# Kernel tuning notes

Measured on AMD Instinct MI355X. Metric: run time of the kernel, lower is better.

Reference implementation:

```python
import jax, jax.numpy as jnp
import numpy as np
import math

B = 50        # graphs per batch
NPG = 2000    # nodes per graph
EPG = 12000   # edges per graph
F_IN = 256
NHID = 128
RATIO = 0.8


def setup_inputs() -> dict:
    key = jax.random.key(0)
    ks = jax.random.split(key, 12)
    N = B * NPG
    src_loc = jax.random.randint(ks[0], (B, EPG), 0, NPG)
    dst_loc = jax.random.randint(ks[1], (B, EPG), 0, NPG)
    off = (jnp.arange(B) * NPG)[:, None]
    edge_index = jnp.stack([(src_loc + off).reshape(-1), (dst_loc + off).reshape(-1)]).astype(jnp.int32)

    def lin(k, fi, fo):
        return (jax.random.normal(k, (fi, fo), jnp.float32) / np.sqrt(fi).astype(np.float32))

    return {
        "x": jax.random.normal(ks[2], (N, F_IN), jnp.float32),
        "W1": lin(ks[3], F_IN, NHID), "b1": jnp.zeros(NHID, jnp.float32),
        "Ws1": lin(ks[4], NHID, 1), "bs1": jnp.zeros(1, jnp.float32),
        "W2": lin(ks[5], NHID, NHID), "b2": jnp.zeros(NHID, jnp.float32),
        "Ws2": lin(ks[6], NHID, 1), "bs2": jnp.zeros(1, jnp.float32),
        "W3": lin(ks[7], NHID, NHID), "b3": jnp.zeros(NHID, jnp.float32),
        "Ws3": lin(ks[8], NHID, 1), "bs3": jnp.zeros(1, jnp.float32),
        "Wl": lin(ks[9], 2 * NHID, NHID), "bl": jnp.zeros(NHID, jnp.float32),
        "edge_index": edge_index,
    }


def gcn_conv(x, W, b, src, dst, w, N):
    # PyG GCNConv: D^{-1/2} (A + I) D^{-1/2} X W + b, deg from edge weights + self loop
    h = x @ W
    deg = jax.ops.segment_sum(w, dst, num_segments=N) + 1.0
    dis = jax.lax.rsqrt(deg)
    norm = w * dis[src] * dis[dst]                       # [E]
    agg = jax.ops.segment_sum(h[src] * norm[:, None], dst, num_segments=N)
    return agg + h / deg[:, None] + b                    # self-loop norm = 1/deg


def sag_pool(x, src, dst, w, Ws, bs, n_per_graph):
    N = x.shape[0]
    k = math.ceil(RATIO * n_per_graph)
    score = gcn_conv(x, Ws, bs, src, dst, w, N)[:, 0]    # [N]
    _, topi = jax.lax.top_k(score.reshape(B, n_per_graph), k)
    perm = (topi + (jnp.arange(B) * n_per_graph)[:, None]).reshape(-1)
    x_new = x[perm] * jnp.tanh(score[perm])[:, None]
    # filter_adj: keep edges whose endpoints survive, reindex; dropped edges -> weight 0
    mapping = jnp.full((N,), -1, jnp.int32).at[perm].set(jnp.arange(B * k, dtype=jnp.int32))
    ns, nd = mapping[src], mapping[dst]
    valid = (ns >= 0) & (nd >= 0) & (w > 0)
    return (x_new, jnp.where(valid, ns, 0), jnp.where(valid, nd, 0),
            jnp.where(valid, w, jnp.zeros((), x.dtype)), k)


def readout(x, n):
    # global max pool || global mean pool (equal-size graphs, nodes grouped per graph)
    xr = x.reshape(B, n, -1)
    return jnp.concatenate([xr.max(axis=1), xr.mean(axis=1)], axis=-1)


def reference(x, W1, b1, Ws1, bs1, W2, b2, Ws2, bs2, W3, b3, Ws3, bs3, Wl, bl, edge_index):
    src, dst = edge_index[0], edge_index[1]
    w = jnp.ones(src.shape[0], x.dtype)
    n = NPG
    x = jax.nn.relu(gcn_conv(x, W1, b1, src, dst, w, B * n))
    x, src, dst, w, n = sag_pool(x, src, dst, w, Ws1, bs1, n)
    x1 = readout(x, n)
    x = jax.nn.relu(gcn_conv(x, W2, b2, src, dst, w, B * n))
    x, src, dst, w, n = sag_pool(x, src, dst, w, Ws2, bs2, n)
    x2 = readout(x, n)
    x = jax.nn.relu(gcn_conv(x, W3, b3, src, dst, w, B * n))
    x, src, dst, w, n = sag_pool(x, src, dst, w, Ws3, bs3, n)
    x3 = readout(x, n)
    return jax.nn.relu((x1 + x2 + x3) @ Wl + bl)
```

## Files before the change

kernel.cpp:

```cpp
#include <hip/hip_runtime.h>
#include <math.h>

#define B_GRAPHS 50
#define NPG0     2000
#define EPG      12000
#define F_IN_C   256
#define NHID     128
#define N0       (B_GRAPHS * NPG0)
#define NE       (B_GRAPHS * EPG)
#define RSEG     16
#define GSLOTS   7
#define CPAD     136

typedef _Float16 f16x8 __attribute__((ext_vector_type(8)));
typedef float    f32x4 __attribute__((ext_vector_type(4)));

static inline int cdiv(int a, int b) { return (a + b - 1) / b; }

__global__ void k_fill_start(int* __restrict__ cnt, float* __restrict__ accum) {
    int i = blockIdx.x * 256 + threadIdx.x;
    if (i < N0) cnt[i] = 0;
    if (i < B_GRAPHS * 256) accum[i] = 0.f;
}

__global__ void k_init_edges(const int* __restrict__ ei, int* __restrict__ esrc,
                             int* __restrict__ edst, float* __restrict__ ew,
                             int* __restrict__ cnt) {
    int e = blockIdx.x * 256 + threadIdx.x;
    if (e < NE) {
        int d = ei[NE + e];
        esrc[e] = ei[e]; edst[e] = d; ew[e] = 1.0f;
        atomicAdd(&cnt[d], 1);
    }
}

__global__ void k_cvt_all(const float* __restrict__ W1, const float* __restrict__ W2,
                          const float* __restrict__ W3, _Float16* __restrict__ WT1,
                          _Float16* __restrict__ WT2, _Float16* __restrict__ WT3) {
    int t = blockIdx.x * 256 + threadIdx.x;
    if (t < 128 * 256) {
        int n = t >> 8, kk = t & 255;
        WT1[t] = (_Float16)W1[kk * 128 + n];
    } else if (t < 128 * 256 + 128 * 128) {
        int u = t - 32768; int n = u >> 7, kk = u & 127;
        WT2[u] = (_Float16)W2[kk * 128 + n];
    } else {
        int u = t - 49152; int n = u >> 7, kk = u & 127;
        WT3[u] = (_Float16)W3[kk * 128 + n];
    }
}

template<int FP32IN, int F, int GATHER>
__global__ __launch_bounds__(256) void k_gemm_ws(const void* __restrict__ Xin,
                                                 const _Float16* __restrict__ WT,
                                                 const int* __restrict__ perm,
                                                 const float* __restrict__ gate,
                                                 _Float16* __restrict__ H, int N) {
    constexpr int SMEMSZ = (F * 128 > 128 * CPAD) ? F * 128 : 128 * CPAD;
    __shared__ _Float16 smem[SMEMSZ];
    const int tid  = threadIdx.x;
    const int wave = tid >> 6, lane = tid & 63;
    const int quad = lane >> 4, l16 = lane & 15;
    const int m_blk = blockIdx.x * 128;

    constexpr int K8 = F / 8;
#pragma unroll
    for (int c = tid; c < 128 * K8; c += 256) {
        int n = c / K8, k8 = c - n * K8;
        f16x8 v = *(const f16x8*)&WT[(size_t)c * 8];
        *(f16x8*)&smem[n * F + ((k8 ^ (n & 7)) << 3)] = v;
    }
    __syncthreads();

    f32x4 acc[2][8];
#pragma unroll
    for (int i = 0; i < 2; ++i)
#pragma unroll
        for (int j = 0; j < 8; ++j) acc[i][j] = {0.f, 0.f, 0.f, 0.f};

    int row0 = m_blk + wave * 32 + l16;
    int row1 = row0 + 16;
    if (row0 > N - 1) row0 = N - 1;
    if (row1 > N - 1) row1 = N - 1;
    _Float16 g0 = (_Float16)1.0f, g1 = (_Float16)1.0f;
    if (GATHER) {
        g0 = (_Float16)gate[row0]; g1 = (_Float16)gate[row1];
        row0 = perm[row0]; row1 = perm[row1];
    }
    const int sx = l16 & 7;
    constexpr int NKQ = F / 32;

    if (FP32IN) {
        constexpr int PD = (NKQ < 4) ? NKQ : 4;
        const float* base0 = (const float*)Xin + (size_t)row0 * F + quad * 8;
        const float* base1 = (const float*)Xin + (size_t)row1 * F + quad * 8;
        float4 p0[PD][2], p1[PD][2];
#pragma unroll
        for (int i = 0; i < PD; ++i) {
            p0[i][0] = ((const float4*)(base0 + i * 32))[0];
            p0[i][1] = ((const float4*)(base0 + i * 32))[1];
            p1[i][0] = ((const float4*)(base1 + i * 32))[0];
            p1[i][1] = ((const float4*)(base1 + i * 32))[1];
        }
#pragma unroll
        for (int kq = 0; kq < NKQ; ++kq) {
            const int b = kq % PD;
            float4 f0 = p0[b][0], f1 = p0[b][1], h0 = p1[b][0], h1 = p1[b][1];
            if (kq + PD < NKQ) {
                p0[b][0] = ((const float4*)(base0 + (kq + PD) * 32))[0];
                p0[b][1] = ((const float4*)(base0 + (kq + PD) * 32))[1];
                p1[b][0] = ((const float4*)(base1 + (kq + PD) * 32))[0];
                p1[b][1] = ((const float4*)(base1 + (kq + PD) * 32))[1];
            }
            f16x8 af0 = (f16x8){(_Float16)f0.x,(_Float16)f0.y,(_Float16)f0.z,(_Float16)f0.w,
                                (_Float16)f1.x,(_Float16)f1.y,(_Float16)f1.z,(_Float16)f1.w};
            f16x8 af1 = (f16x8){(_Float16)h0.x,(_Float16)h0.y,(_Float16)h0.z,(_Float16)h0.w,
                                (_Float16)h1.x,(_Float16)h1.y,(_Float16)h1.z,(_Float16)h1.w};
            f16x8 bf[8];
#pragma unroll
            for (int j = 0; j < 8; ++j)
                bf[j] = *(const f16x8*)&smem[(j * 16 + l16) * F + ((((kq << 2) + quad) ^ sx) << 3)];
#pragma unroll
            for (int j = 0; j < 8; ++j) {
                acc[0][j] = __builtin_amdgcn_mfma_f32_16x16x32_f16(af0, bf[j], acc[0][j], 0, 0, 0);
                acc[1][j] = __builtin_amdgcn_mfma_f32_16x16x32_f16(af1, bf[j], acc[1][j], 0, 0, 0);
            }
        }
    } else {
        const _Float16* base0 = (const _Float16*)Xin + (size_t)row0 * F + quad * 8;
        const _Float16* base1 = (const _Float16*)Xin + (size_t)row1 * F + quad * 8;
        f16x8 q0[NKQ], q1[NKQ];
#pragma unroll
        for (int i = 0; i < NKQ; ++i) {
            q0[i] = *(const f16x8*)(base0 + i * 32);
            q1[i] = *(const f16x8*)(base1 + i * 32);
        }
#pragma unroll
        for (int kq = 0; kq < NKQ; ++kq) {
            f16x8 af0 = q0[kq], af1 = q1[kq];
            if (GATHER) { af0 = af0 * g0; af1 = af1 * g1; }
            f16x8 bf[8];
#pragma unroll
            for (int j = 0; j < 8; ++j)
                bf[j] = *(const f16x8*)&smem[(j * 16 + l16) * F + ((((kq << 2) + quad) ^ sx) << 3)];
#pragma unroll
            for (int j = 0; j < 8; ++j) {
                acc[0][j] = __builtin_amdgcn_mfma_f32_16x16x32_f16(af0, bf[j], acc[0][j], 0, 0, 0);
                acc[1][j] = __builtin_amdgcn_mfma_f32_16x16x32_f16(af1, bf[j], acc[1][j], 0, 0, 0);
            }
        }
    }
    __syncthreads();

    _Float16* sC = smem;
    const int rw = wave * 32;
#pragma unroll
    for (int i = 0; i < 2; ++i)
#pragma unroll
        for (int j = 0; j < 8; ++j)
#pragma unroll
            for (int g = 0; g < 4; ++g)
                sC[(rw + i * 16 + quad * 4 + g) * CPAD + j * 16 + l16] = (_Float16)acc[i][j][g];
    __syncthreads();
    {
        int rr = tid >> 1;
        int gr = m_blk + rr;
        if (gr < N) {
            _Float16* Hr = H + (size_t)gr * 128 + (tid & 1) * 64;
            const _Float16* Sr = sC + rr * CPAD + (tid & 1) * 64;
#pragma unroll
            for (int c = 0; c < 8; ++c)
                *(f16x8*)&Hr[c * 8] = *(const f16x8*)&Sr[c * 8];
        }
    }
}

__global__ __launch_bounds__(256) void k_scan(const int* __restrict__ cnt,
                                              int* __restrict__ offs,
                                              int* __restrict__ cursor, int npg) {
    __shared__ int ch[256];
    int b = blockIdx.x, tid = threadIdx.x;
    int per = (npg + 255) >> 8;
    int base = b * npg;
    int s0 = tid * per;
    int s1 = s0 + per; if (s1 > npg) s1 = npg; if (s0 > npg) s0 = npg;
    int s = 0;
    for (int i = s0; i < s1; ++i) s += cnt[base + i];
    ch[tid] = s;
    __syncthreads();
    for (int d = 1; d < 256; d <<= 1) {
        int t = ch[tid] + ((tid >= d) ? ch[tid - d] : 0);
        __syncthreads();
        ch[tid] = t;
        __syncthreads();
    }
    int run = b * EPG + ch[tid] - s;
    for (int i = s0; i < s1; ++i) {
        offs[base + i] = run; cursor[base + i] = run;
        run += cnt[base + i];
    }
}

__global__ void k_fill_csr(const int* __restrict__ esrc, const int* __restrict__ edst,
                           const float* __restrict__ ew, const int* __restrict__ cnt,
                           int* __restrict__ cursor, int* __restrict__ csr_src,
                           float* __restrict__ csr_norm) {
    int e = blockIdx.x * 256 + threadIdx.x;
    if (e < NE) {
        if (ew[e] > 0.f) {
            int sN = esrc[e], d = edst[e];
            int pos = atomicAdd(&cursor[d], 1);
            csr_src[pos] = sN;
            csr_norm[pos] = rsqrtf((float)(cnt[sN] + 1)) * rsqrtf((float)(cnt[d] + 1));
        }
    }
}

__global__ __launch_bounds__(256) void k_agg(const _Float16* __restrict__ H,
                                             const int* __restrict__ csr_src,
                                             const float* __restrict__ csr_norm,
                                             const int* __restrict__ offs,
                                             const int* __restrict__ cnt,
                                             const float* __restrict__ bias,
                                             const float* __restrict__ Ws,
                                             _Float16* __restrict__ X,
                                             float* __restrict__ hs,
                                             int bpg, int npg) {
    int bi = blockIdx.x;
    int x = bi & 7, s = bi >> 3;
    int gslot = s / bpg, blk = s - gslot * bpg;
    int g = x + 8 * gslot;
    if (g >= B_GRAPHS) return;
    int node = g * npg + blk * 4 + (threadIdx.x >> 6);
    int lane = threadIdx.x & 63;
    int quad = lane >> 4, l16 = lane & 15;

    int st = offs[node], c = cnt[node], en = st + c;
    float acc[8];
#pragma unroll
    for (int j = 0; j < 8; ++j) acc[j] = 0.f;

    if (c > 0) {
        for (int e0 = st; e0 < en; e0 += 8) {
            int eA = e0 + quad, eB = eA + 4;
            int ecA = eA < en ? eA : en - 1;
            int ecB = eB < en ? eB : en - 1;
            int uA = csr_src[ecA], uB = csr_src[ecB];
            float nA = (eA < en) ? csr_norm[ecA] : 0.f;
            float nB = (eB < en) ? csr_norm[ecB] : 0.f;
            f16x8 hA = *(const f16x8*)&H[(size_t)uA * NHID + l16 * 8];
            f16x8 hB = *(const f16x8*)&H[(size_t)uB * NHID + l16 * 8];
#pragma unroll
            for (int j = 0; j < 8; ++j) acc[j] = fmaf((float)hA[j], nA, acc[j]);
#pragma unroll
            for (int j = 0; j < 8; ++j) acc[j] = fmaf((float)hB[j], nB, acc[j]);
        }
    }
#pragma unroll
    for (int j = 0; j < 8; ++j) {
        acc[j] += __shfl_xor(acc[j], 16, 64);
        acc[j] += __shfl_xor(acc[j], 32, 64);
    }
    float invd = 1.f / (float)(c + 1);
    f16x8 hn = *(const f16x8*)&H[(size_t)node * NHID + l16 * 8];
    float4 b0 = *(const float4*)&bias[l16 * 8];
    float4 b1 = *(const float4*)&bias[l16 * 8 + 4];
    float4 w0 = *(const float4*)&Ws[l16 * 8];
    float4 w1 = *(const float4*)&Ws[l16 * 8 + 4];
    const float bb[8] = {b0.x, b0.y, b0.z, b0.w, b1.x, b1.y, b1.z, b1.w};
    const float ww[8] = {w0.x, w0.y, w0.z, w0.w, w1.x, w1.y, w1.z, w1.w};
    float sd = 0.f;
    f16x8 o;
#pragma unroll
    for (int j = 0; j < 8; ++j) {
        float v = fmaxf(acc[j] + (float)hn[j] * invd + bb[j], 0.f);
        o[j] = (_Float16)v;
        sd = fmaf(v, ww[j], sd);
    }
    if (quad == 0)
        *(f16x8*)&X[(size_t)node * NHID + l16 * 8] = o;
    sd += __shfl_xor(sd, 1, 64);
    sd += __shfl_xor(sd, 2, 64);
    sd += __shfl_xor(sd, 4, 64);
    sd += __shfl_xor(sd, 8, 64);
    if (lane == 0) hs[node] = sd;
}

__global__ void k_score(const float* __restrict__ hs, const int* __restrict__ csr_src,
                        const float* __restrict__ csr_norm, const int* __restrict__ offs,
                        const int* __restrict__ cnt, const float* __restrict__ bs,
                        float* __restrict__ score, int N) {
    int i = blockIdx.x * 256 + threadIdx.x;
    if (i >= N) return;
    int s = offs[i], c = cnt[i];
    float a = 0.f;
    for (int e = s; e < s + c; ++e) a = fmaf(hs[csr_src[e]], csr_norm[e], a);
    score[i] = a + hs[i] / (float)(c + 1) + bs[0];
}

__global__ __launch_bounds__(1024) void k_topk(const float* __restrict__ score,
                                               int* __restrict__ mapping,
                                               int* __restrict__ perm,
                                               float* __restrict__ gate,
                                               int* __restrict__ cntN,
                                               int npg, int k) {
    __shared__ float ss[2048];
    __shared__ int   si[2048];
    int b = blockIdx.x, tid = threadIdx.x;
    for (int i = tid; i < 2048; i += 1024) {
        if (i < npg) { ss[i] = score[b * npg + i]; si[i] = i; }
        else         { ss[i] = -__builtin_inff();  si[i] = i; }
    }
    __syncthreads();
    for (int size = 2; size <= 2048; size <<= 1) {
        for (int stride = size >> 1; stride > 0; stride >>= 1) {
            int t = tid;
            int i = ((t & ~(stride - 1)) << 1) | (t & (stride - 1));
            int j = i | stride;
            float sa = ss[i], sb = ss[j];
            int   ia = si[i], ib = si[j];
            bool b_before_a = (sb > sa) || (sb == sa && ib < ia);
            bool forward = ((i & size) == 0);
            bool doswap = forward ? b_before_a : !b_before_a;
            if (doswap) { ss[i] = sb; ss[j] = sa; si[i] = ib; si[j] = ia; }
            __syncthreads();
        }
    }
    for (int j = tid; j < npg; j += 1024) {
        int oldg = b * npg + si[j];
        if (j < k) {
            int newg = b * k + j;
            perm[newg] = oldg;
            mapping[oldg] = newg;
            gate[newg] = tanhf(ss[j]);
        } else {
            mapping[oldg] = -1;
        }
    }
    for (int j = tid; j < k; j += 1024) cntN[b * k + j] = 0;
}

__global__ __launch_bounds__(128) void k_pool_readout(const _Float16* __restrict__ X,
                                                      const float* __restrict__ gate,
                                                      const int* __restrict__ perm,
                                                      float* __restrict__ pmax,
                                                      float* __restrict__ psum, int k) {
    int s = blockIdx.x, b = blockIdx.y, f = threadIdx.x;
    int j0 = (k * s) / RSEG, j1 = (k * (s + 1)) / RSEG;
    float mx = -__builtin_inff(), sm = 0.f;
    for (int j = j0; j < j1; ++j) {
        int g = b * k + j;
        int old = perm[g];
        float v = (float)X[(size_t)old * NHID + f] * gate[g];
        mx = fmaxf(mx, v);
        sm += v;
    }
    pmax[(size_t)(b * RSEG + s) * NHID + f] = mx;
    psum[(size_t)(b * RSEG + s) * NHID + f] = sm;
}

__global__ __launch_bounds__(128) void k_readout_comb(const float* __restrict__ pmax,
                                                      const float* __restrict__ psum,
                                                      float* __restrict__ accum, int k) {
    int b = blockIdx.x, f = threadIdx.x;
    float mx = -__builtin_inff(), sm = 0.f;
#pragma unroll
    for (int s = 0; s < RSEG; ++s) {
        mx = fmaxf(mx, pmax[(size_t)(b * RSEG + s) * NHID + f]);
        sm += psum[(size_t)(b * RSEG + s) * NHID + f];
    }
    accum[b * 256 + f]       += mx;
    accum[b * 256 + 128 + f] += sm / (float)k;
}

__global__ void k_remap(int* __restrict__ esrc, int* __restrict__ edst,
                        float* __restrict__ ew, const int* __restrict__ mapping,
                        int* __restrict__ cntN) {
    int e = blockIdx.x * 256 + threadIdx.x;
    if (e >= NE) return;
    int sN = esrc[e], d = edst[e];
    float we = ew[e];
    int ns = mapping[sN], nd = mapping[d];
    bool valid = (ns >= 0) && (nd >= 0) && (we > 0.f);
    esrc[e] = valid ? ns : 0;
    edst[e] = valid ? nd : 0;
    ew[e] = valid ? we : 0.f;
    if (valid) atomicAdd(&cntN[nd], 1);
}

__global__ __launch_bounds__(128) void k_comb_final(const float* __restrict__ pmax,
                                                    const float* __restrict__ psum,
                                                    const float* __restrict__ accum,
                                                    const float* __restrict__ Wl,
                                                    const float* __restrict__ bl,
                                                    float* __restrict__ out, int k) {
    __shared__ float a[256];
    int b = blockIdx.x, f = threadIdx.x;
    float mx = -__builtin_inff(), sm = 0.f;
#pragma unroll
    for (int s = 0; s < RSEG; ++s) {
        mx = fmaxf(mx, pmax[(size_t)(b * RSEG + s) * NHID + f]);
        sm += psum[(size_t)(b * RSEG + s) * NHID + f];
    }
    a[f]       = accum[b * 256 + f] + mx;
    a[128 + f] = accum[b * 256 + 128 + f] + sm / (float)k;
    __syncthreads();
    float s = bl[f];
    for (int i = 0; i < 256; ++i) s = fmaf(a[i], Wl[i * NHID + f], s);
    out[b * NHID + f] = fmaxf(s, 0.f);
}

extern "C" void kernel_launch(void* const* d_in, const int* in_sizes, int n_in,
                              void* d_out, int out_size, void* d_ws, size_t ws_size,
                              hipStream_t stream) {
    const float* x0 = (const float*)d_in[0];
    const float* Wm[3] = {(const float*)d_in[1], (const float*)d_in[5], (const float*)d_in[9]};
    const float* bm[3] = {(const float*)d_in[2], (const float*)d_in[6], (const float*)d_in[10]};
    const float* Wsc[3] = {(const float*)d_in[3], (const float*)d_in[7], (const float*)d_in[11]};
    const float* bsc[3] = {(const float*)d_in[4], (const float*)d_in[8], (const float*)d_in[12]};
    const float* Wl = (const float*)d_in[13];
    const float* bl = (const float*)d_in[14];
    const int*   ei = (const int*)d_in[15];
    float* out = (float*)d_out;

    _Float16* bufA = (_Float16*)d_ws;
    _Float16* bufB = bufA + (size_t)N0 * NHID;
    _Float16* WT1  = bufB + (size_t)N0 * NHID;
    _Float16* WT2  = WT1 + 128 * 256;
    _Float16* WT3  = WT2 + 128 * 128;
    float* hs     = (float*)(WT3 + 128 * 128);
    float* score  = hs + N0;
    float* gate   = score + N0;
    float* accum  = gate + N0;
    float* pmax   = accum + B_GRAPHS * 256;
    float* psum   = pmax + B_GRAPHS * RSEG * NHID;
    int*   cntA   = (int*)(psum + B_GRAPHS * RSEG * NHID);
    int*   cntB   = cntA + N0;
    int*   offs   = cntB + N0;
    int*   cursor = offs + N0;
    int*   mapping= cursor + N0;
    int*   perm   = mapping + N0;
    int*   esrc   = perm + N0;
    int*   edst   = esrc + NE;
    float* ew     = (float*)(edst + NE);
    int*   csr_src= (int*)(ew + NE);
    float* csr_norm = (float*)(csr_src + NE);

    _Float16* WTs[3] = {WT1, WT2, WT3};
    const int EG = cdiv(NE, 256);

    k_fill_start<<<cdiv(N0, 256), 256, 0, stream>>>(cntA, accum);
    k_init_edges<<<EG, 256, 0, stream>>>(ei, esrc, edst, ew, cntA);
    k_cvt_all<<<256, 256, 0, stream>>>(Wm[0], Wm[1], Wm[2], WT1, WT2, WT3);

    int npg = NPG0;
    _Float16* Hbuf = bufA; _Float16* Xbuf = bufB;

    for (int layer = 0; layer < 3; ++layer) {
        int N = B_GRAPHS * npg;
        int k = (npg * 4) / 5;
        int NG = cdiv(N, 256);
        int bpg = npg >> 2;
        int* cnt  = (layer == 1) ? cntB : cntA;
        int* cntN = (layer == 1) ? cntA : cntB;

        if (layer == 0)
            k_gemm_ws<1, 256, 0><<<cdiv(N, 128), 256, 0, stream>>>(x0, WTs[0], perm, gate, Hbuf, N);
        else
            k_gemm_ws<0, 128, 1><<<cdiv(N, 128), 256, 0, stream>>>(Xbuf, WTs[layer], perm, gate, Hbuf, N);
        k_scan<<<B_GRAPHS, 256, 0, stream>>>(cnt, offs, cursor, npg);
        k_fill_csr<<<EG, 256, 0, stream>>>(esrc, edst, ew, cnt, cursor, csr_src, csr_norm);
        k_agg<<<8 * GSLOTS * bpg, 256, 0, stream>>>(Hbuf, csr_src, csr_norm, offs, cnt,
                                                    bm[layer], Wsc[layer], Xbuf, hs, bpg, npg);
        k_score<<<NG, 256, 0, stream>>>(hs, csr_src, csr_norm, offs, cnt, bsc[layer], score, N);
        k_topk<<<B_GRAPHS, 1024, 0, stream>>>(score, mapping, perm, gate, cntN, npg, k);
        k_pool_readout<<<dim3(RSEG, B_GRAPHS), 128, 0, stream>>>(Xbuf, gate, perm, pmax, psum, k);
        if (layer < 2) {
            k_remap<<<EG, 256, 0, stream>>>(esrc, edst, ew, mapping, cntN);
            k_readout_comb<<<B_GRAPHS, 128, 0, stream>>>(pmax, psum, accum, k);
        } else {
            k_comb_final<<<B_GRAPHS, 128, 0, stream>>>(pmax, psum, accum, Wl, bl, out, k);
        }

        npg = k;
    }
}
```

Baseline: 642.1 us.

## Fuse scan with CSR fill, score into topk, and read GEMM weights from global

```diff
diff --git a/kernel.cpp b/kernel.cpp
--- a/kernel.cpp
+++ b/kernel.cpp
@@ -51,26 +51,16 @@
 }
 
 template<int FP32IN, int F, int GATHER>
-__global__ __launch_bounds__(256) void k_gemm_ws(const void* __restrict__ Xin,
+__global__ __launch_bounds__(256) void k_gemm_gb(const void* __restrict__ Xin,
                                                  const _Float16* __restrict__ WT,
                                                  const int* __restrict__ perm,
                                                  const float* __restrict__ gate,
                                                  _Float16* __restrict__ H, int N) {
-    constexpr int SMEMSZ = (F * 128 > 128 * CPAD) ? F * 128 : 128 * CPAD;
-    __shared__ _Float16 smem[SMEMSZ];
+    __shared__ _Float16 smem[4 * 32 * CPAD];
     const int tid  = threadIdx.x;
     const int wave = tid >> 6, lane = tid & 63;
     const int quad = lane >> 4, l16 = lane & 15;
     const int m_blk = blockIdx.x * 128;
-
-    constexpr int K8 = F / 8;
-#pragma unroll
-    for (int c = tid; c < 128 * K8; c += 256) {
-        int n = c / K8, k8 = c - n * K8;
-        f16x8 v = *(const f16x8*)&WT[(size_t)c * 8];
-        *(f16x8*)&smem[n * F + ((k8 ^ (n & 7)) << 3)] = v;
-    }
-    __syncthreads();
 
     f32x4 acc[2][8];
 #pragma unroll
@@ -87,11 +77,11 @@
         g0 = (_Float16)gate[row0]; g1 = (_Float16)gate[row1];
         row0 = perm[row0]; row1 = perm[row1];
     }
-    const int sx = l16 & 7;
     constexpr int NKQ = F / 32;
+    const _Float16* WTb = WT + l16 * F + quad * 8;
 
     if (FP32IN) {
-        constexpr int PD = (NKQ < 4) ? NKQ : 4;
+        constexpr int PD = 2;
         const float* base0 = (const float*)Xin + (size_t)row0 * F + quad * 8;
         const float* base1 = (const float*)Xin + (size_t)row1 * F + quad * 8;
         float4 p0[PD][2], p1[PD][2];
@@ -119,7 +109,7 @@
             f16x8 bf[8];
 #pragma unroll
             for (int j = 0; j < 8; ++j)
-                bf[j] = *(const f16x8*)&smem[(j * 16 + l16) * F + ((((kq << 2) + quad) ^ sx) << 3)];
+                bf[j] = *(const f16x8*)&WTb[j * 16 * F + kq * 32];
 #pragma unroll
             for (int j = 0; j < 8; ++j) {
                 acc[0][j] = __builtin_amdgcn_mfma_f32_16x16x32_f16(af0, bf[j], acc[0][j], 0, 0, 0);
@@ -142,7 +132,7 @@
             f16x8 bf[8];
 #pragma unroll
             for (int j = 0; j < 8; ++j)
-                bf[j] = *(const f16x8*)&smem[(j * 16 + l16) * F + ((((kq << 2) + quad) ^ sx) << 3)];
+                bf[j] = *(const f16x8*)&WTb[j * 16 * F + kq * 32];
 #pragma unroll
             for (int j = 0; j < 8; ++j) {
                 acc[0][j] = __builtin_amdgcn_mfma_f32_16x16x32_f16(af0, bf[j], acc[0][j], 0, 0, 0);
@@ -150,24 +140,21 @@
             }
         }
     }
-    __syncthreads();
-
-    _Float16* sC = smem;
-    const int rw = wave * 32;
+
+    _Float16* sC = smem + wave * 32 * CPAD;
 #pragma unroll
     for (int i = 0; i < 2; ++i)
 #pragma unroll
         for (int j = 0; j < 8; ++j)
 #pragma unroll
             for (int g = 0; g < 4; ++g)
-                sC[(rw + i * 16 + quad * 4 + g) * CPAD + j * 16 + l16] = (_Float16)acc[i][j][g];
-    __syncthreads();
+                sC[(i * 16 + quad * 4 + g) * CPAD + j * 16 + l16] = (_Float16)acc[i][j][g];
     {
-        int rr = tid >> 1;
-        int gr = m_blk + rr;
+        int rl = lane >> 1;
+        int gr = m_blk + wave * 32 + rl;
         if (gr < N) {
-            _Float16* Hr = H + (size_t)gr * 128 + (tid & 1) * 64;
-            const _Float16* Sr = sC + rr * CPAD + (tid & 1) * 64;
+            _Float16* Hr = H + (size_t)gr * 128 + (lane & 1) * 64;
+            const _Float16* Sr = sC + rl * CPAD + (lane & 1) * 64;
 #pragma unroll
             for (int c = 0; c < 8; ++c)
                 *(f16x8*)&Hr[c * 8] = *(const f16x8*)&Sr[c * 8];
@@ -175,20 +162,24 @@
     }
 }
 
-__global__ __launch_bounds__(256) void k_scan(const int* __restrict__ cnt,
-                                              int* __restrict__ offs,
-                                              int* __restrict__ cursor, int npg) {
-    __shared__ int ch[256];
+__global__ __launch_bounds__(1024) void k_scan_csr(const int* __restrict__ cnt,
+                                                   int* __restrict__ offs,
+                                                   const int* __restrict__ esrc,
+                                                   const int* __restrict__ edst,
+                                                   const float* __restrict__ ew,
+                                                   int* __restrict__ csr_src,
+                                                   float* __restrict__ csr_norm, int npg) {
+    __shared__ int ch[1024];
+    __shared__ int lcur[2048];
     int b = blockIdx.x, tid = threadIdx.x;
-    int per = (npg + 255) >> 8;
     int base = b * npg;
-    int s0 = tid * per;
-    int s1 = s0 + per; if (s1 > npg) s1 = npg; if (s0 > npg) s0 = npg;
+    int s0 = tid * 2, s1 = s0 + 2;
+    if (s1 > npg) s1 = npg; if (s0 > npg) s0 = npg;
     int s = 0;
     for (int i = s0; i < s1; ++i) s += cnt[base + i];
     ch[tid] = s;
     __syncthreads();
-    for (int d = 1; d < 256; d <<= 1) {
+    for (int d = 1; d < 1024; d <<= 1) {
         int t = ch[tid] + ((tid >= d) ? ch[tid - d] : 0);
         __syncthreads();
         ch[tid] = t;
@@ -196,20 +187,14 @@
     }
     int run = b * EPG + ch[tid] - s;
     for (int i = s0; i < s1; ++i) {
-        offs[base + i] = run; cursor[base + i] = run;
+        offs[base + i] = run; lcur[i] = run;
         run += cnt[base + i];
     }
-}
-
-__global__ void k_fill_csr(const int* __restrict__ esrc, const int* __restrict__ edst,
-                           const float* __restrict__ ew, const int* __restrict__ cnt,
-                           int* __restrict__ cursor, int* __restrict__ csr_src,
-                           float* __restrict__ csr_norm) {
-    int e = blockIdx.x * 256 + threadIdx.x;
-    if (e < NE) {
+    __syncthreads();
+    for (int e = b * EPG + tid; e < (b + 1) * EPG; e += 1024) {
         if (ew[e] > 0.f) {
             int sN = esrc[e], d = edst[e];
-            int pos = atomicAdd(&cursor[d], 1);
+            int pos = atomicAdd(&lcur[d - base], 1);
             csr_src[pos] = sN;
             csr_norm[pos] = rsqrtf((float)(cnt[sN] + 1)) * rsqrtf((float)(cnt[d] + 1));
         }
@@ -286,19 +271,12 @@
     if (lane == 0) hs[node] = sd;
 }
 
-__global__ void k_score(const float* __restrict__ hs, const int* __restrict__ csr_src,
-                        const float* __restrict__ csr_norm, const int* __restrict__ offs,
-                        const int* __restrict__ cnt, const float* __restrict__ bs,
-                        float* __restrict__ score, int N) {
-    int i = blockIdx.x * 256 + threadIdx.x;
-    if (i >= N) return;
-    int s = offs[i], c = cnt[i];
-    float a = 0.f;
-    for (int e = s; e < s + c; ++e) a = fmaf(hs[csr_src[e]], csr_norm[e], a);
-    score[i] = a + hs[i] / (float)(c + 1) + bs[0];
-}
-
-__global__ __launch_bounds__(1024) void k_topk(const float* __restrict__ score,
+__global__ __launch_bounds__(1024) void k_topk(const float* __restrict__ hs,
+                                               const int* __restrict__ csr_src,
+                                               const float* __restrict__ csr_norm,
+                                               const int* __restrict__ offs,
+                                               const int* __restrict__ cnt,
+                                               const float* __restrict__ bs,
                                                int* __restrict__ mapping,
                                                int* __restrict__ perm,
                                                float* __restrict__ gate,
@@ -307,9 +285,17 @@
     __shared__ float ss[2048];
     __shared__ int   si[2048];
     int b = blockIdx.x, tid = threadIdx.x;
+    float bias0 = bs[0];
     for (int i = tid; i < 2048; i += 1024) {
-        if (i < npg) { ss[i] = score[b * npg + i]; si[i] = i; }
-        else         { ss[i] = -__builtin_inff();  si[i] = i; }
+        if (i < npg) {
+            int node = b * npg + i;
+            int st = offs[node], c = cnt[node];
+            float a = 0.f;
+            for (int e = st; e < st + c; ++e)
+                a = fmaf(hs[csr_src[e]], csr_norm[e], a);
+            ss[i] = a + hs[node] / (float)(c + 1) + bias0;
+            si[i] = i;
+        } else { ss[i] = -__builtin_inff(); si[i] = i; }
     }
     __syncthreads();
     for (int size = 2; size <= 2048; size <<= 1) {
@@ -429,16 +415,14 @@
     _Float16* WT2  = WT1 + 128 * 256;
     _Float16* WT3  = WT2 + 128 * 128;
     float* hs     = (float*)(WT3 + 128 * 128);
-    float* score  = hs + N0;
-    float* gate   = score + N0;
+    float* gate   = hs + N0;
     float* accum  = gate + N0;
     float* pmax   = accum + B_GRAPHS * 256;
     float* psum   = pmax + B_GRAPHS * RSEG * NHID;
     int*   cntA   = (int*)(psum + B_GRAPHS * RSEG * NHID);
     int*   cntB   = cntA + N0;
     int*   offs   = cntB + N0;
-    int*   cursor = offs + N0;
-    int*   mapping= cursor + N0;
+    int*   mapping= offs + N0;
     int*   perm   = mapping + N0;
     int*   esrc   = perm + N0;
     int*   edst   = esrc + NE;
@@ -459,21 +443,19 @@
     for (int layer = 0; layer < 3; ++layer) {
         int N = B_GRAPHS * npg;
         int k = (npg * 4) / 5;
-        int NG = cdiv(N, 256);
         int bpg = npg >> 2;
         int* cnt  = (layer == 1) ? cntB : cntA;
         int* cntN = (layer == 1) ? cntA : cntB;
 
         if (layer == 0)
-            k_gemm_ws<1, 256, 0><<<cdiv(N, 128), 256, 0, stream>>>(x0, WTs[0], perm, gate, Hbuf, N);
+            k_gemm_gb<1, 256, 0><<<cdiv(N, 128), 256, 0, stream>>>(x0, WTs[0], perm, gate, Hbuf, N);
         else
-            k_gemm_ws<0, 128, 1><<<cdiv(N, 128), 256, 0, stream>>>(Xbuf, WTs[layer], perm, gate, Hbuf, N);
-        k_scan<<<B_GRAPHS, 256, 0, stream>>>(cnt, offs, cursor, npg);
-        k_fill_csr<<<EG, 256, 0, stream>>>(esrc, edst, ew, cnt, cursor, csr_src, csr_norm);
+            k_gemm_gb<0, 128, 1><<<cdiv(N, 128), 256, 0, stream>>>(Xbuf, WTs[layer], perm, gate, Hbuf, N);
+        k_scan_csr<<<B_GRAPHS, 1024, 0, stream>>>(cnt, offs, esrc, edst, ew, csr_src, csr_norm, npg);
         k_agg<<<8 * GSLOTS * bpg, 256, 0, stream>>>(Hbuf, csr_src, csr_norm, offs, cnt,
                                                     bm[layer], Wsc[layer], Xbuf, hs, bpg, npg);
-        k_score<<<NG, 256, 0, stream>>>(hs, csr_src, csr_norm, offs, cnt, bsc[layer], score, N);
-        k_topk<<<B_GRAPHS, 1024, 0, stream>>>(score, mapping, perm, gate, cntN, npg, k);
+        k_topk<<<B_GRAPHS, 1024, 0, stream>>>(hs, csr_src, csr_norm, offs, cnt, bsc[layer],
+                                              mapping, perm, gate, cntN, npg, k);
         k_pool_readout<<<dim3(RSEG, B_GRAPHS), 128, 0, stream>>>(Xbuf, gate, perm, pmax, psum, k);
         if (layer < 2) {
             k_remap<<<EG, 256, 0, stream>>>(esrc, edst, ew, mapping, cntN);
```

Result: slower. 673.4 us (+4.9%).

## Shrink GEMM tile to 64 rows and read weights directly from global

Applied to the files above, without the earlier changes.

```diff
diff --git a/kernel.cpp b/kernel.cpp
--- a/kernel.cpp
+++ b/kernel.cpp
@@ -51,125 +51,88 @@
 }
 
 template<int FP32IN, int F, int GATHER>
-__global__ __launch_bounds__(256) void k_gemm_ws(const void* __restrict__ Xin,
-                                                 const _Float16* __restrict__ WT,
-                                                 const int* __restrict__ perm,
-                                                 const float* __restrict__ gate,
-                                                 _Float16* __restrict__ H, int N) {
-    constexpr int SMEMSZ = (F * 128 > 128 * CPAD) ? F * 128 : 128 * CPAD;
-    __shared__ _Float16 smem[SMEMSZ];
+__global__ __launch_bounds__(256) void k_gemm64(const void* __restrict__ Xin,
+                                                const _Float16* __restrict__ WT,
+                                                const int* __restrict__ perm,
+                                                const float* __restrict__ gate,
+                                                _Float16* __restrict__ H, int N) {
+    __shared__ _Float16 smem[4 * 16 * CPAD];
     const int tid  = threadIdx.x;
     const int wave = tid >> 6, lane = tid & 63;
     const int quad = lane >> 4, l16 = lane & 15;
-    const int m_blk = blockIdx.x * 128;
-
-    constexpr int K8 = F / 8;
-#pragma unroll
-    for (int c = tid; c < 128 * K8; c += 256) {
-        int n = c / K8, k8 = c - n * K8;
-        f16x8 v = *(const f16x8*)&WT[(size_t)c * 8];
-        *(f16x8*)&smem[n * F + ((k8 ^ (n & 7)) << 3)] = v;
-    }
-    __syncthreads();
-
-    f32x4 acc[2][8];
-#pragma unroll
-    for (int i = 0; i < 2; ++i)
-#pragma unroll
-        for (int j = 0; j < 8; ++j) acc[i][j] = {0.f, 0.f, 0.f, 0.f};
-
-    int row0 = m_blk + wave * 32 + l16;
-    int row1 = row0 + 16;
-    if (row0 > N - 1) row0 = N - 1;
-    if (row1 > N - 1) row1 = N - 1;
-    _Float16 g0 = (_Float16)1.0f, g1 = (_Float16)1.0f;
-    if (GATHER) {
-        g0 = (_Float16)gate[row0]; g1 = (_Float16)gate[row1];
-        row0 = perm[row0]; row1 = perm[row1];
-    }
-    const int sx = l16 & 7;
+    const int m_blk = blockIdx.x * 64;
+
+    f32x4 acc[8];
+#pragma unroll
+    for (int j = 0; j < 8; ++j) acc[j] = {0.f, 0.f, 0.f, 0.f};
+
+    int row = m_blk + wave * 16 + l16;
+    if (row > N - 1) row = N - 1;
+    _Float16 gt = (_Float16)1.0f;
+    if (GATHER) { gt = (_Float16)gate[row]; row = perm[row]; }
     constexpr int NKQ = F / 32;
+    const _Float16* WTb = WT + l16 * F + quad * 8;
 
     if (FP32IN) {
         constexpr int PD = (NKQ < 4) ? NKQ : 4;
-        const float* base0 = (const float*)Xin + (size_t)row0 * F + quad * 8;
-        const float* base1 = (const float*)Xin + (size_t)row1 * F + quad * 8;
-        float4 p0[PD][2], p1[PD][2];
+        const float* base = (const float*)Xin + (size_t)row * F + quad * 8;
+        float4 p[PD][2];
 #pragma unroll
         for (int i = 0; i < PD; ++i) {
-            p0[i][0] = ((const float4*)(base0 + i * 32))[0];
-            p0[i][1] = ((const float4*)(base0 + i * 32))[1];
-            p1[i][0] = ((const float4*)(base1 + i * 32))[0];
-            p1[i][1] = ((const float4*)(base1 + i * 32))[1];
+            p[i][0] = ((const float4*)(base + i * 32))[0];
+            p[i][1] = ((const float4*)(base + i * 32))[1];
         }
 #pragma unroll
         for (int kq = 0; kq < NKQ; ++kq) {
             const int b = kq % PD;
-            float4 f0 = p0[b][0], f1 = p0[b][1], h0 = p1[b][0], h1 = p1[b][1];
+            float4 f0 = p[b][0], f1 = p[b][1];
             if (kq + PD < NKQ) {
-                p0[b][0] = ((const float4*)(base0 + (kq + PD) * 32))[0];
-                p0[b][1] = ((const float4*)(base0 + (kq + PD) * 32))[1];
-                p1[b][0] = ((const float4*)(base1 + (kq + PD) * 32))[0];
-                p1[b][1] = ((const float4*)(base1 + (kq + PD) * 32))[1];
+                p[b][0] = ((const float4*)(base + (kq + PD) * 32))[0];
+                p[b][1] = ((const float4*)(base + (kq + PD) * 32))[1];
             }
-            f16x8 af0 = (f16x8){(_Float16)f0.x,(_Float16)f0.y,(_Float16)f0.z,(_Float16)f0.w,
-                                (_Float16)f1.x,(_Float16)f1.y,(_Float16)f1.z,(_Float16)f1.w};
-            f16x8 af1 = (f16x8){(_Float16)h0.x,(_Float16)h0.y,(_Float16)h0.z,(_Float16)h0.w,
-                                (_Float16)h1.x,(_Float16)h1.y,(_Float16)h1.z,(_Float16)h1.w};
+            f16x8 af = (f16x8){(_Float16)f0.x,(_Float16)f0.y,(_Float16)f0.z,(_Float16)f0.w,
+                               (_Float16)f1.x,(_Float16)f1.y,(_Float16)f1.z,(_Float16)f1.w};
             f16x8 bf[8];
 #pragma unroll
             for (int j = 0; j < 8; ++j)
-                bf[j] = *(const f16x8*)&smem[(j * 16 + l16) * F + ((((kq << 2) + quad) ^ sx) << 3)];
-#pragma unroll
-            for (int j = 0; j < 8; ++j) {
-                acc[0][j] = __builtin_amdgcn_mfma_f32_16x16x32_f16(af0, bf[j], acc[0][j], 0, 0, 0);
-                acc[1][j] = __builtin_amdgcn_mfma_f32_16x16x32_f16(af1, bf[j], acc[1][j], 0, 0, 0);
-            }
+                bf[j] = *(const f16x8*)&WTb[j * 16 * F + kq * 32];
+#pragma unroll
+            for (int j = 0; j < 8; ++j)
+                acc[j] = __builtin_amdgcn_mfma_f32_16x16x32_f16(af, bf[j], acc[j], 0, 0, 0);
         }
     } else {
-        const _Float16* base0 = (const _Float16*)Xin + (size_t)row0 * F + quad * 8;
-        const _Float16* base1 = (const _Float16*)Xin + (size_t)row1 * F + quad * 8;
-        f16x8 q0[NKQ], q1[NKQ];
-#pragma unroll
-        for (int i = 0; i < NKQ; ++i) {
-            q0[i] = *(const f16x8*)(base0 + i * 32);
-            q1[i] = *(const f16x8*)(base1 + i * 32);
-        }
+        const _Float16* base = (const _Float16*)Xin + (size_t)row * F + quad * 8;
+        f16x8 q[NKQ];
+#pragma unroll
+        for (int i = 0; i < NKQ; ++i) q[i] = *(const f16x8*)(base + i * 32);
 #pragma unroll
         for (int kq = 0; kq < NKQ; ++kq) {
-            f16x8 af0 = q0[kq], af1 = q1[kq];
-            if (GATHER) { af0 = af0 * g0; af1 = af1 * g1; }
+            f16x8 af = q[kq];
+            if (GATHER) af = af * gt;
             f16x8 bf[8];
 #pragma unroll
             for (int j = 0; j < 8; ++j)
-                bf[j] = *(const f16x8*)&smem[(j * 16 + l16) * F + ((((kq << 2) + quad) ^ sx) << 3)];
-#pragma unroll
-            for (int j = 0; j < 8; ++j) {
-                acc[0][j] = __builtin_amdgcn_mfma_f32_16x16x32_f16(af0, bf[j], acc[0][j], 0, 0, 0);
-                acc[1][j] = __builtin_amdgcn_mfma_f32_16x16x32_f16(af1, bf[j], acc[1][j], 0, 0, 0);
-            }
-        }
-    }
-    __syncthreads();
-
-    _Float16* sC = smem;
-    const int rw = wave * 32;
-#pragma unroll
-    for (int i = 0; i < 2; ++i)
-#pragma unroll
-        for (int j = 0; j < 8; ++j)
-#pragma unroll
-            for (int g = 0; g < 4; ++g)
-                sC[(rw + i * 16 + quad * 4 + g) * CPAD + j * 16 + l16] = (_Float16)acc[i][j][g];
-    __syncthreads();
+                bf[j] = *(const f16x8*)&WTb[j * 16 * F + kq * 32];
+#pragma unroll
+            for (int j = 0; j < 8; ++j)
+                acc[j] = __builtin_amdgcn_mfma_f32_16x16x32_f16(af, bf[j], acc[j], 0, 0, 0);
+        }
+    }
+
+    _Float16* sC = smem + wave * 16 * CPAD;
+#pragma unroll
+    for (int j = 0; j < 8; ++j)
+#pragma unroll
+        for (int g = 0; g < 4; ++g)
+            sC[(quad * 4 + g) * CPAD + j * 16 + l16] = (_Float16)acc[j][g];
     {
-        int rr = tid >> 1;
-        int gr = m_blk + rr;
+        int rl = lane >> 2;
+        int gr = m_blk + wave * 16 + rl;
         if (gr < N) {
-            _Float16* Hr = H + (size_t)gr * 128 + (tid & 1) * 64;
-            const _Float16* Sr = sC + rr * CPAD + (tid & 1) * 64;
-#pragma unroll
-            for (int c = 0; c < 8; ++c)
+            _Float16* Hr = H + (size_t)gr * 128 + (lane & 3) * 32;
+            const _Float16* Sr = sC + rl * CPAD + (lane & 3) * 32;
+#pragma unroll
+            for (int c = 0; c < 4; ++c)
                 *(f16x8*)&Hr[c * 8] = *(const f16x8*)&Sr[c * 8];
         }
     }
@@ -465,9 +428,9 @@
         int* cntN = (layer == 1) ? cntA : cntB;
 
         if (layer == 0)
-            k_gemm_ws<1, 256, 0><<<cdiv(N, 128), 256, 0, stream>>>(x0, WTs[0], perm, gate, Hbuf, N);
+            k_gemm64<1, 256, 0><<<cdiv(N, 64), 256, 0, stream>>>(x0, WTs[0], perm, gate, Hbuf, N);
         else
-            k_gemm_ws<0, 128, 1><<<cdiv(N, 128), 256, 0, stream>>>(Xbuf, WTs[layer], perm, gate, Hbuf, N);
+            k_gemm64<0, 128, 1><<<cdiv(N, 64), 256, 0, stream>>>(Xbuf, WTs[layer], perm, gate, Hbuf, N);
         k_scan<<<B_GRAPHS, 256, 0, stream>>>(cnt, offs, cursor, npg);
         k_fill_csr<<<EG, 256, 0, stream>>>(esrc, edst, ew, cnt, cursor, csr_src, csr_norm);
         k_agg<<<8 * GSLOTS * bpg, 256, 0, stream>>>(Hbuf, csr_src, csr_norm, offs, cnt,
```

Result: slower. 690.8 us (+7.6%).
